# Optimization experiments

Hardware: AMD Instinct MI355X
Metric: run time of the kernel (lower is better)

The kernel has to match this reference:

```python
import jax, jax.numpy as jnp
import numpy as np

N_EXPERTS = 8
TOP_K = 2


def setup_inputs() -> dict:
    key = jax.random.key(0)
    ks = jax.random.split(key, 5)
    B, T, C, E, H = 8, 2048, 256, 8, 682  # H = int(8/3*256)
    scale = 1.0 / np.sqrt(C)
    return {
        "x": jax.random.normal(ks[0], (B, T, C), dtype=jnp.float32),
        "router_w": jax.random.normal(ks[1], (E, C), dtype=jnp.float32) * scale,
        "w1": jax.random.normal(ks[2], (E, H, C), dtype=jnp.float32) * scale,
        "w2": jax.random.normal(ks[3], (E, C, H), dtype=jnp.float32) * (1.0 / np.sqrt(H)),
        "w3": jax.random.normal(ks[4], (E, H, C), dtype=jnp.float32) * scale,
    }


def reference(x, router_w, w1, w2, w3):
    B, T, C = x.shape
    flat = x.reshape(-1, C)  # [N, C]

    # Router: softmax over experts, top-k selection, renormalize.
    logits = flat @ router_w.T                     # [N, E]
    probs = jax.nn.softmax(logits, axis=-1)
    topk_probs, topk_idx = jax.lax.top_k(probs, TOP_K)
    topk_probs = topk_probs / (jnp.sum(topk_probs, axis=-1, keepdims=True) + 1e-9)

    # Dense gate matrix [N, E]: zero for non-selected experts (same math as
    # the masked loop, since unselected experts contribute weight 0).
    onehot = jax.nn.one_hot(topk_idx, N_EXPERTS, dtype=flat.dtype)  # [N, K, E]
    gates = jnp.einsum("nk,nke->ne", topk_probs, onehot)           # [N, E]

    # SwiGLU experts, computed densely over E and combined with gates.
    h1 = jnp.einsum("nc,ehc->neh", flat, w1)       # [N, E, H]
    h3 = jnp.einsum("nc,ehc->neh", flat, w3)       # [N, E, H]
    h = jax.nn.silu(h1) * h3                       # [N, E, H]
    y = jnp.einsum("neh,ech->nec", h, w2)          # [N, E, C]
    out = jnp.einsum("ne,nec->nc", gates, y)       # [N, C]
    return out.reshape(B, T, C)
```

## Files before the change

kernel.cpp:

```cpp
#include <hip/hip_runtime.h>
#include <hip/hip_bf16.h>

#define N_TOK 16384
#define C_DIM 256
#define E_NUM 8
#define H_DIM 682
#define H_PAD 768
#define NROWS (N_TOK * 2)
#define HB 64
#define APB (NROWS / HB)
#define MAXTILE 264

typedef short short8 __attribute__((ext_vector_type(8)));
typedef float floatx4 __attribute__((ext_vector_type(4)));
typedef unsigned int uint;

__device__ inline unsigned short f2bf(float v) {
    union { float f; uint u; } x; x.f = v;
    uint r = (x.u + 0x7fffu + ((x.u >> 16) & 1u)) >> 16;
    return (unsigned short)r;
}
__device__ inline float bf2f(unsigned short v) {
    union { uint u; float f; } x; x.u = ((uint)v) << 16; return x.f;
}
__device__ inline uint pk2(float a, float b) {
    return (uint)f2bf(a) | ((uint)f2bf(b) << 16);
}

__device__ __forceinline__ void load_lds16(const void* g, void* l) {
    __builtin_amdgcn_global_load_lds(
        (const __attribute__((address_space(1))) unsigned int*)g,
        (__attribute__((address_space(3))) unsigned int*)l, 16, 0, 0);
}

#define VMCNT8 asm volatile("s_waitcnt vmcnt(8)" ::: "memory")
#define VMCNT6 asm volatile("s_waitcnt vmcnt(6)" ::: "memory")
#define VMCNT0 asm volatile("s_waitcnt vmcnt(0)" ::: "memory")
#define LGKM0  asm volatile("s_waitcnt lgkmcnt(0)" ::: "memory")

#define P13 (E_NUM * H_PAD * (C_DIM / 2))
#define P2  (E_NUM * C_DIM * (H_PAD / 2))
#define NQUAD ((2 * P13 + P2) / 4)
#define WCONV_BLKS (NQUAD / 256)
#define Q13 (P13 / 4)

__global__ __launch_bounds__(256) void prep_kernel(
    const float* __restrict__ w1, const float* __restrict__ w3, const float* __restrict__ w2,
    unsigned short* __restrict__ w1b, unsigned short* __restrict__ w3b,
    unsigned short* __restrict__ w2b,
    const float* __restrict__ x, const float* __restrict__ rw,
    unsigned short* __restrict__ xb, int* __restrict__ as_e, float* __restrict__ as_gate) {
    __shared__ float rws[E_NUM * C_DIM];
    int tid = threadIdx.x;
    if (blockIdx.x < WCONV_BLKS) {
        int q = blockIdx.x * 256 + tid;
        if (q < 2 * Q13) {
            const float* src = (q < Q13) ? w1 : w3;
            unsigned short* dst = (q < Q13) ? w1b : w3b;
            int i4 = (q < Q13) ? q : q - Q13;
            int e = i4 / (H_PAD * 32);
            int rem = i4 - e * (H_PAD * 32);
            int r = rem >> 5;
            int qc = rem & 31;
            int4 v = {0, 0, 0, 0};
            if (r < H_DIM) {
                const float* s = src + ((size_t)e * H_DIM + r) * C_DIM + qc * 8;
                float4 f0 = *(const float4*)s;
                float4 f1 = *(const float4*)(s + 4);
                v.x = pk2(f0.x, f0.y); v.y = pk2(f0.z, f0.w);
                v.z = pk2(f1.x, f1.y); v.w = pk2(f1.z, f1.w);
            }
            *(int4*)((uint*)dst + (size_t)i4 * 4) = v;
        } else {
            int i4 = q - 2 * Q13;
            int e = i4 / (C_DIM * 96);
            int rem = i4 - e * (C_DIM * 96);
            int r = rem / 96;
            int qc = rem - r * 96;
            const float* s = w2 + ((size_t)e * C_DIM + r) * H_DIM;
            int4 v = {0, 0, 0, 0};
            int j0 = qc * 4;
#pragma unroll
            for (int k = 0; k < 4; k++) {
                int j = j0 + k;
                if (j * 2 < H_DIM) {
                    float2 f = *(const float2*)(s + j * 2);
                    ((uint*)&v)[k] = pk2(f.x, f.y);
                }
            }
            *(int4*)((uint*)w2b + (size_t)i4 * 4) = v;
        }
        return;
    }
    for (int i = tid; i < E_NUM * C_DIM; i += 256) rws[i] = rw[i];
    __syncthreads();
    int wave = tid >> 6, lane = tid & 63;
    int t = (blockIdx.x - WCONV_BLKS) * 4 + wave;
    const float4 xv = *(const float4*)(x + (size_t)t * C_DIM + lane * 4);
    uint2 pk;
    pk.x = pk2(xv.x, xv.y);
    pk.y = pk2(xv.z, xv.w);
    *(uint2*)(xb + (size_t)t * C_DIM + lane * 4) = pk;
    float p[E_NUM];
#pragma unroll
    for (int e = 0; e < E_NUM; e++) {
        const float* wr = &rws[e * C_DIM + lane * 4];
        p[e] = xv.x * wr[0] + xv.y * wr[1] + xv.z * wr[2] + xv.w * wr[3];
    }
#pragma unroll
    for (int off = 32; off >= 1; off >>= 1) {
#pragma unroll
        for (int e = 0; e < E_NUM; e++) p[e] += __shfl_down(p[e], off, 64);
    }
    if (lane == 0) {
        float m = p[0];
#pragma unroll
        for (int e = 1; e < E_NUM; e++) m = fmaxf(m, p[e]);
        float s = 0.f, q[E_NUM];
#pragma unroll
        for (int e = 0; e < E_NUM; e++) { q[e] = expf(p[e] - m); s += q[e]; }
#pragma unroll
        for (int e = 0; e < E_NUM; e++) q[e] /= s;
        int e0 = 0;
#pragma unroll
        for (int e = 1; e < E_NUM; e++) if (q[e] > q[e0]) e0 = e;
        int e1 = (e0 == 0) ? 1 : 0;
#pragma unroll
        for (int e = 0; e < E_NUM; e++) {
            if (e != e0 && q[e] > q[e1]) e1 = e;
        }
        float g0 = q[e0], g1 = q[e1];
        float denom = g0 + g1 + 1e-9f;
        g0 /= denom; g1 /= denom;
        as_e[t * 2] = e0; as_gate[t * 2] = g0;
        as_e[t * 2 + 1] = e1; as_gate[t * 2 + 1] = g1;
    }
}

__global__ __launch_bounds__(256) void hist_kernel(const int* __restrict__ as_e,
                                                   int* __restrict__ block_hist) {
    __shared__ int lh[E_NUM];
    int b = blockIdx.x, tid = threadIdx.x;
    if (tid < E_NUM) lh[tid] = 0;
    __syncthreads();
    for (int i = tid; i < APB; i += 256) atomicAdd(&lh[as_e[b * APB + i]], 1);
    __syncthreads();
    if (tid < E_NUM) block_hist[b * E_NUM + tid] = lh[tid];
}

__global__ void scan2_kernel(const int* __restrict__ block_hist, int* __restrict__ offsets,
                             int* __restrict__ block_base, int* __restrict__ tile_base) {
    __shared__ int tot[E_NUM], off[E_NUM];
    int e = threadIdx.x;
    if (e < E_NUM) {
        int s = 0;
        for (int b = 0; b < HB; b++) s += block_hist[b * E_NUM + e];
        tot[e] = s;
    }
    __syncthreads();
    if (e == 0) {
        int acc = 0;
        for (int i = 0; i < E_NUM; i++) { off[i] = acc; offsets[i] = acc; acc += tot[i]; }
        offsets[E_NUM] = acc;
        int t = 0;
        tile_base[0] = 0;
        for (int i = 0; i < E_NUM; i++) { t += (tot[i] + 127) / 128; tile_base[i + 1] = t; }
    }
    __syncthreads();
    if (e < E_NUM) {
        int acc = off[e];
        for (int b = 0; b < HB; b++) { block_base[b * E_NUM + e] = acc; acc += block_hist[b * E_NUM + e]; }
    }
}

__global__ __launch_bounds__(256) void scatter_kernel(
    const int* __restrict__ as_e, const int* __restrict__ block_base,
    int* __restrict__ row_token, int* __restrict__ as_row) {
    __shared__ int cur[E_NUM];
    int b = blockIdx.x, tid = threadIdx.x;
    if (tid < E_NUM) cur[tid] = block_base[b * E_NUM + tid];
    __syncthreads();
    for (int i = tid; i < APB; i += 256) {
        int a = b * APB + i;
        int e = as_e[a];
        int p = atomicAdd(&cur[e], 1);
        row_token[p] = a >> 1;
        as_row[a] = p;
    }
}

__device__ __forceinline__ int tile_to_expert(const int* __restrict__ tile_base, int bid) {
    int e = 0;
#pragma unroll
    for (int i = 1; i < E_NUM; i++) e += (bid >= tile_base[i]) ? 1 : 0;
    return e;
}

__global__ __launch_bounds__(256, 2) void expert_ffn1(
    const unsigned short* __restrict__ xb, const unsigned short* __restrict__ w1b,
    const unsigned short* __restrict__ w3b, const int* __restrict__ offsets,
    const int* __restrict__ tile_base, const int* __restrict__ row_token,
    unsigned short* __restrict__ h) {
    int bid = blockIdx.x;
    int xcd = bid & 7;
    int local = bid >> 3;
    int tq = local / 6;
    int c = local - tq * 6;
    int t = tq * 8 + xcd;
    if (t >= tile_base[E_NUM]) return;
    int e = tile_to_expert(tile_base, t);
    int mt = t - tile_base[e];
    int off0 = offsets[e], off1 = offsets[e + 1];
    int row0 = off0 + mt * 128;
    int mval = min(128, off1 - row0);

    __shared__ union {
        unsigned short buf[3][12288];
        unsigned short Hs[128 * 136];
    } sm;

    int tid = threadIdx.x, lane = tid & 63, w = tid >> 6;
    int wm = w & 1, wn = w >> 1;
    int ra = tid >> 2;
    int acol = (((tid & 3) ^ ((ra >> 1) & 3))) * 8;
    int tok0 = row_token[row0 + min(ra, mval - 1)];
    int tok1 = row_token[row0 + min(ra + 64, mval - 1)];
    const unsigned short* a0p = xb + (size_t)tok0 * C_DIM + acol;
    const unsigned short* a1p = xb + (size_t)tok1 * C_DIM + acol;
    const unsigned short* b1p0 = w1b + ((size_t)e * H_PAD + c * 128 + ra) * C_DIM + acol;
    const unsigned short* b1p1 = b1p0 + (size_t)64 * C_DIM;
    const unsigned short* b3p0 = w3b + ((size_t)e * H_PAD + c * 128 + ra) * C_DIM + acol;
    const unsigned short* b3p1 = b3p0 + (size_t)64 * C_DIM;

    int wofs = w * 512;
    auto stageA = [&](int kt, unsigned short* base) {
        int kb = kt * 32;
        load_lds16(a0p + kb, base + wofs);
        load_lds16(a1p + kb, base + 2048 + wofs);
        load_lds16(b1p0 + kb, base + 4096 + wofs);
    };
    auto stageB = [&](int kt, unsigned short* base) {
        int kb = kt * 32;
        load_lds16(b1p1 + kb, base + 6144 + wofs);
        load_lds16(b3p0 + kb, base + 8192 + wofs);
        load_lds16(b3p1 + kb, base + 10240 + wofs);
    };

    int ko = ((lane >> 4) ^ ((lane >> 1) & 3)) * 8;
    int l15 = lane & 15;
    int arowf = wm * 64 + l15;
    int browf = wn * 64 + l15;
    int quad = lane >> 4;

    stageA(0, sm.buf[0]); stageB(0, sm.buf[0]);
    stageA(1, sm.buf[1]); stageB(1, sm.buf[1]);

    floatx4 acc1[4][4], acc3[4][4];
#pragma unroll
    for (int m = 0; m < 4; m++)
#pragma unroll
        for (int n = 0; n < 4; n++) {
            acc1[m][n] = (floatx4){0.f, 0.f, 0.f, 0.f};
            acc3[m][n] = (floatx4){0.f, 0.f, 0.f, 0.f};
        }

#pragma unroll
    for (int kt = 0; kt < 8; kt++) {
        if (kt < 7) { VMCNT6; } else { VMCNT0; }
        __builtin_amdgcn_s_barrier();
        const unsigned short* cur = sm.buf[kt % 3];
        unsigned short* nbuf = sm.buf[(kt + 2) % 3];
        short8 af[4], b1f[4], b3f[4];
#pragma unroll
        for (int m = 0; m < 4; m++) af[m] = *(short8*)&cur[(arowf + m * 16) * 32 + ko];
#pragma unroll
        for (int n = 0; n < 4; n++) b1f[n] = *(short8*)&cur[4096 + (browf + n * 16) * 32 + ko];
        if (kt + 2 < 8) stageA(kt + 2, nbuf);
#pragma unroll
        for (int n = 0; n < 4; n++) b3f[n] = *(short8*)&cur[8192 + (browf + n * 16) * 32 + ko];
        __builtin_amdgcn_s_setprio(1);
#pragma unroll
        for (int m = 0; m < 4; m++)
#pragma unroll
            for (int n = 0; n < 4; n++)
                acc1[m][n] = __builtin_amdgcn_mfma_f32_16x16x32_bf16(af[m], b1f[n], acc1[m][n], 0, 0, 0);
        __builtin_amdgcn_s_setprio(0);
        __builtin_amdgcn_s_barrier();
        if (kt + 2 < 8) stageB(kt + 2, nbuf);
        __builtin_amdgcn_s_setprio(1);
#pragma unroll
        for (int m = 0; m < 4; m++)
#pragma unroll
            for (int n = 0; n < 4; n++)
                acc3[m][n] = __builtin_amdgcn_mfma_f32_16x16x32_bf16(af[m], b3f[n], acc3[m][n], 0, 0, 0);
        __builtin_amdgcn_s_setprio(0);
        __builtin_amdgcn_s_barrier();
    }
    __syncthreads();

#pragma unroll
    for (int m = 0; m < 4; m++)
#pragma unroll
        for (int n = 0; n < 4; n++)
#pragma unroll
            for (int r = 0; r < 4; r++) {
                float h1 = acc1[m][n][r], h3 = acc3[m][n][r];
                float sv = h1 / (1.0f + __expf(-h1)) * h3;
                sm.Hs[(wm * 64 + m * 16 + quad * 4 + r) * 136 + wn * 64 + n * 16 + l15] = f2bf(sv);
            }
    __syncthreads();
#pragma unroll
    for (int it = 0; it < 8; it++) {
        int s = it * 256 + tid;
        int row = s >> 4, c16 = s & 15;
        if (row < mval)
            *(int4*)(h + (size_t)(row0 + row) * H_PAD + c * 128 + c16 * 8) =
                *(int4*)&sm.Hs[row * 136 + c16 * 8];
    }
}

__global__ __launch_bounds__(256, 2) void expert_ffn2(
    const unsigned short* __restrict__ h, const unsigned short* __restrict__ w2b,
    const int* __restrict__ offsets, const int* __restrict__ tile_base,
    unsigned short* __restrict__ y) {
    int bid = blockIdx.x;
    int xcd = bid & 7;
    int local = bid >> 3;
    int tq = local >> 1;
    int p = local & 1;
    int t = tq * 8 + xcd;
    if (t >= tile_base[E_NUM]) return;
    int e = tile_to_expert(tile_base, t);
    int mt = t - tile_base[e];
    int off0 = offsets[e], off1 = offsets[e + 1];
    int row0 = off0 + mt * 128;
    int mval = min(128, off1 - row0);

    __shared__ union {
        unsigned short buf[2][16384];
        unsigned short Hs[128 * 136];
    } sm;

    int tid = threadIdx.x, lane = tid & 63, w = tid >> 6;
    int wm = w & 1, wn = w >> 1;
    int ra = tid >> 2;
    int acol = (((tid & 3) ^ ((ra >> 1) & 3))) * 8;
    const unsigned short* ap0 = h + (size_t)(row0 + ra) * H_PAD + acol;
    const unsigned short* ap1 = ap0 + (size_t)64 * H_PAD;
    const unsigned short* bp0 = w2b + ((size_t)e * C_DIM + p * 128 + ra) * H_PAD + acol;
    const unsigned short* bp1 = bp0 + (size_t)64 * H_PAD;

    int wofs = w * 512;
    auto stage = [&](int kt, unsigned short* base) {
        int kb = kt * 64;
#pragma unroll
        for (int kk = 0; kk < 2; kk++) {
            int ks = kb + kk * 32;
            unsigned short* b2 = base + kk * 8192;
            load_lds16(ap0 + ks, b2 + wofs);
            load_lds16(ap1 + ks, b2 + 2048 + wofs);
            load_lds16(bp0 + ks, b2 + 4096 + wofs);
            load_lds16(bp1 + ks, b2 + 6144 + wofs);
        }
    };

    int ko = ((lane >> 4) ^ ((lane >> 1) & 3)) * 8;
    int l15 = lane & 15;
    int arowf = wm * 64 + l15;
    int browf = wn * 64 + l15;
    int quad = lane >> 4;

    stage(0, sm.buf[0]);

    floatx4 acc[4][4];
#pragma unroll
    for (int m = 0; m < 4; m++)
#pragma unroll
        for (int n = 0; n < 4; n++) acc[m][n] = (floatx4){0.f, 0.f, 0.f, 0.f};

#pragma unroll
    for (int kt = 0; kt < H_PAD / 64; kt++) {
        if (kt + 1 < H_PAD / 64) stage(kt + 1, sm.buf[(kt + 1) & 1]);
        if (kt + 1 < H_PAD / 64) { VMCNT8; } else { VMCNT0; }
        __builtin_amdgcn_s_barrier();
        const unsigned short* cur = sm.buf[kt & 1];
#pragma unroll
        for (int kk = 0; kk < 2; kk++) {
            const unsigned short* c2 = cur + kk * 8192;
            short8 af[4], bf[4];
#pragma unroll
            for (int m = 0; m < 4; m++) af[m] = *(short8*)&c2[(arowf + m * 16) * 32 + ko];
#pragma unroll
            for (int n = 0; n < 4; n++) bf[n] = *(short8*)&c2[4096 + (browf + n * 16) * 32 + ko];
            __builtin_amdgcn_s_setprio(1);
#pragma unroll
            for (int m = 0; m < 4; m++)
#pragma unroll
                for (int n = 0; n < 4; n++)
                    acc[m][n] = __builtin_amdgcn_mfma_f32_16x16x32_bf16(af[m], bf[n], acc[m][n], 0, 0, 0);
            __builtin_amdgcn_s_setprio(0);
        }
        LGKM0;
        __builtin_amdgcn_s_barrier();
    }
    __syncthreads();

#pragma unroll
    for (int m = 0; m < 4; m++)
#pragma unroll
        for (int n = 0; n < 4; n++)
#pragma unroll
            for (int r = 0; r < 4; r++)
                sm.Hs[(wm * 64 + m * 16 + quad * 4 + r) * 136 + wn * 64 + n * 16 + l15] =
                    f2bf(acc[m][n][r]);
    __syncthreads();
#pragma unroll
    for (int it = 0; it < 8; it++) {
        int s = it * 256 + tid;
        int row = s >> 4, c16 = s & 15;
        if (row < mval)
            *(int4*)(y + (size_t)(row0 + row) * C_DIM + p * 128 + c16 * 8) =
                *(int4*)&sm.Hs[row * 136 + c16 * 8];
    }
}

__global__ __launch_bounds__(256) void combine_kernel(
    const unsigned short* __restrict__ y, const int* __restrict__ as_row,
    const float* __restrict__ as_gate, float* __restrict__ out) {
    int tid = threadIdx.x, lane = tid & 63;
    int t = blockIdx.x * 4 + (tid >> 6);
    int r0 = as_row[2 * t], r1 = as_row[2 * t + 1];
    float g0 = as_gate[2 * t], g1 = as_gate[2 * t + 1];
    uint2 a = *(const uint2*)(y + (size_t)r0 * C_DIM + lane * 4);
    uint2 b = *(const uint2*)(y + (size_t)r1 * C_DIM + lane * 4);
    float4 o;
    o.x = g0 * bf2f((unsigned short)(a.x & 0xffff)) + g1 * bf2f((unsigned short)(b.x & 0xffff));
    o.y = g0 * bf2f((unsigned short)(a.x >> 16)) + g1 * bf2f((unsigned short)(b.x >> 16));
    o.z = g0 * bf2f((unsigned short)(a.y & 0xffff)) + g1 * bf2f((unsigned short)(b.y & 0xffff));
    o.w = g0 * bf2f((unsigned short)(a.y >> 16)) + g1 * bf2f((unsigned short)(b.y >> 16));
    *(float4*)(out + (size_t)t * C_DIM + lane * 4) = o;
}

extern "C" void kernel_launch(void* const* d_in, const int* in_sizes, int n_in,
                              void* d_out, int out_size, void* d_ws, size_t ws_size,
                              hipStream_t stream) {
    const float* x = (const float*)d_in[0];
    const float* rw = (const float*)d_in[1];
    const float* w1 = (const float*)d_in[2];
    const float* w2 = (const float*)d_in[3];
    const float* w3 = (const float*)d_in[4];
    float* out = (float*)d_out;

    char* ws = (char*)d_ws;
    size_t o = 0;
    auto alloc = [&](size_t bytes) {
        void* p = ws + o;
        o = (o + bytes + 255) & ~(size_t)255;
        return p;
    };
    unsigned short* xb = (unsigned short*)alloc((size_t)N_TOK * C_DIM * 2);
    unsigned short* w1b = (unsigned short*)alloc((size_t)E_NUM * H_PAD * C_DIM * 2);
    unsigned short* w3b = (unsigned short*)alloc((size_t)E_NUM * H_PAD * C_DIM * 2);
    unsigned short* w2b = (unsigned short*)alloc((size_t)E_NUM * C_DIM * H_PAD * 2);
    unsigned short* hbuf = (unsigned short*)alloc((size_t)(NROWS + 128) * H_PAD * 2);
    unsigned short* ybuf = (unsigned short*)alloc((size_t)NROWS * C_DIM * 2);
    int* offsets = (int*)alloc((E_NUM + 1) * 4);
    int* tile_base = (int*)alloc((E_NUM + 1) * 4);
    int* as_e = (int*)alloc(NROWS * 4);
    float* as_gate = (float*)alloc(NROWS * 4);
    int* row_token = (int*)alloc(NROWS * 4);
    int* as_row = (int*)alloc(NROWS * 4);
    int* block_hist = (int*)alloc(HB * E_NUM * 4);
    int* block_base = (int*)alloc(HB * E_NUM * 4);

    prep_kernel<<<WCONV_BLKS + N_TOK / 4, 256, 0, stream>>>(
        w1, w3, w2, w1b, w3b, w2b, x, rw, xb, as_e, as_gate);
    hist_kernel<<<HB, 256, 0, stream>>>(as_e, block_hist);
    scan2_kernel<<<1, 64, 0, stream>>>(block_hist, offsets, block_base, tile_base);
    scatter_kernel<<<HB, 256, 0, stream>>>(as_e, block_base, row_token, as_row);

    expert_ffn1<<<6 * MAXTILE, 256, 0, stream>>>(xb, w1b, w3b, offsets, tile_base,
                                                 row_token, hbuf);
    expert_ffn2<<<2 * MAXTILE, 256, 0, stream>>>(hbuf, w2b, offsets, tile_base, ybuf);
    combine_kernel<<<N_TOK / 4, 256, 0, stream>>>(ybuf, as_row, as_gate, out);
}
```

Measured before the change: 176.9 us.

## Fold scan into scatter kernel and process four tokens per wave in prep

Removes the single-block scan kernel: each scatter block now recomputes the per-expert totals and its own prefix from block_hist, and block 0 writes offsets and tile_base. This drops one kernel launch and the serial scan dependency. Separately, the router/prep blocks now handle four tokens per wave, cutting block count by 4x and amortizing the router-weight LDS load. The cost is redundant prefix work in every scatter block and a longer serial loop per routing block.

```diff
diff --git a/kernel.cpp b/kernel.cpp
--- a/kernel.cpp
+++ b/kernel.cpp
@@ -95,45 +95,49 @@
     for (int i = tid; i < E_NUM * C_DIM; i += 256) rws[i] = rw[i];
     __syncthreads();
     int wave = tid >> 6, lane = tid & 63;
-    int t = (blockIdx.x - WCONV_BLKS) * 4 + wave;
-    const float4 xv = *(const float4*)(x + (size_t)t * C_DIM + lane * 4);
-    uint2 pk;
-    pk.x = pk2(xv.x, xv.y);
-    pk.y = pk2(xv.z, xv.w);
-    *(uint2*)(xb + (size_t)t * C_DIM + lane * 4) = pk;
-    float p[E_NUM];
-#pragma unroll
-    for (int e = 0; e < E_NUM; e++) {
-        const float* wr = &rws[e * C_DIM + lane * 4];
-        p[e] = xv.x * wr[0] + xv.y * wr[1] + xv.z * wr[2] + xv.w * wr[3];
-    }
-#pragma unroll
-    for (int off = 32; off >= 1; off >>= 1) {
-#pragma unroll
-        for (int e = 0; e < E_NUM; e++) p[e] += __shfl_down(p[e], off, 64);
-    }
-    if (lane == 0) {
-        float m = p[0];
-#pragma unroll
-        for (int e = 1; e < E_NUM; e++) m = fmaxf(m, p[e]);
-        float s = 0.f, q[E_NUM];
-#pragma unroll
-        for (int e = 0; e < E_NUM; e++) { q[e] = expf(p[e] - m); s += q[e]; }
-#pragma unroll
-        for (int e = 0; e < E_NUM; e++) q[e] /= s;
-        int e0 = 0;
-#pragma unroll
-        for (int e = 1; e < E_NUM; e++) if (q[e] > q[e0]) e0 = e;
-        int e1 = (e0 == 0) ? 1 : 0;
+    int tbase = (blockIdx.x - WCONV_BLKS) * 16 + wave * 4;
+#pragma unroll
+    for (int tt = 0; tt < 4; tt++) {
+        int t = tbase + tt;
+        const float4 xv = *(const float4*)(x + (size_t)t * C_DIM + lane * 4);
+        uint2 pk;
+        pk.x = pk2(xv.x, xv.y);
+        pk.y = pk2(xv.z, xv.w);
+        *(uint2*)(xb + (size_t)t * C_DIM + lane * 4) = pk;
+        float p[E_NUM];
 #pragma unroll
         for (int e = 0; e < E_NUM; e++) {
-            if (e != e0 && q[e] > q[e1]) e1 = e;
-        }
-        float g0 = q[e0], g1 = q[e1];
-        float denom = g0 + g1 + 1e-9f;
-        g0 /= denom; g1 /= denom;
-        as_e[t * 2] = e0; as_gate[t * 2] = g0;
-        as_e[t * 2 + 1] = e1; as_gate[t * 2 + 1] = g1;
+            const float* wr = &rws[e * C_DIM + lane * 4];
+            p[e] = xv.x * wr[0] + xv.y * wr[1] + xv.z * wr[2] + xv.w * wr[3];
+        }
+#pragma unroll
+        for (int off = 32; off >= 1; off >>= 1) {
+#pragma unroll
+            for (int e = 0; e < E_NUM; e++) p[e] += __shfl_down(p[e], off, 64);
+        }
+        if (lane == 0) {
+            float m = p[0];
+#pragma unroll
+            for (int e = 1; e < E_NUM; e++) m = fmaxf(m, p[e]);
+            float s = 0.f, q[E_NUM];
+#pragma unroll
+            for (int e = 0; e < E_NUM; e++) { q[e] = expf(p[e] - m); s += q[e]; }
+#pragma unroll
+            for (int e = 0; e < E_NUM; e++) q[e] /= s;
+            int e0 = 0;
+#pragma unroll
+            for (int e = 1; e < E_NUM; e++) if (q[e] > q[e0]) e0 = e;
+            int e1 = (e0 == 0) ? 1 : 0;
+#pragma unroll
+            for (int e = 0; e < E_NUM; e++) {
+                if (e != e0 && q[e] > q[e1]) e1 = e;
+            }
+            float g0 = q[e0], g1 = q[e1];
+            float denom = g0 + g1 + 1e-9f;
+            g0 /= denom; g1 /= denom;
+            as_e[t * 2] = e0; as_gate[t * 2] = g0;
+            as_e[t * 2 + 1] = e1; as_gate[t * 2 + 1] = g1;
+        }
     }
 }
 
@@ -148,37 +152,37 @@
     if (tid < E_NUM) block_hist[b * E_NUM + tid] = lh[tid];
 }
 
-__global__ void scan2_kernel(const int* __restrict__ block_hist, int* __restrict__ offsets,
-                             int* __restrict__ block_base, int* __restrict__ tile_base) {
-    __shared__ int tot[E_NUM], off[E_NUM];
-    int e = threadIdx.x;
-    if (e < E_NUM) {
-        int s = 0;
-        for (int b = 0; b < HB; b++) s += block_hist[b * E_NUM + e];
-        tot[e] = s;
-    }
-    __syncthreads();
-    if (e == 0) {
+__global__ __launch_bounds__(256) void scatter_kernel(
+    const int* __restrict__ as_e, const int* __restrict__ block_hist,
+    int* __restrict__ offsets, int* __restrict__ tile_base,
+    int* __restrict__ row_token, int* __restrict__ as_row) {
+    __shared__ int tot_s[E_NUM], pre_s[E_NUM], off_s[E_NUM], cur[E_NUM];
+    int b = blockIdx.x, tid = threadIdx.x;
+    if (tid < E_NUM) {
+        int e = tid, tot = 0, pre = 0;
+        for (int bb = 0; bb < HB; bb++) {
+            int v = block_hist[bb * E_NUM + e];
+            if (bb < b) pre += v;
+            tot += v;
+        }
+        tot_s[e] = tot; pre_s[e] = pre;
+    }
+    __syncthreads();
+    if (tid == 0) {
         int acc = 0;
-        for (int i = 0; i < E_NUM; i++) { off[i] = acc; offsets[i] = acc; acc += tot[i]; }
-        offsets[E_NUM] = acc;
-        int t = 0;
-        tile_base[0] = 0;
-        for (int i = 0; i < E_NUM; i++) { t += (tot[i] + 127) / 128; tile_base[i + 1] = t; }
-    }
-    __syncthreads();
-    if (e < E_NUM) {
-        int acc = off[e];
-        for (int b = 0; b < HB; b++) { block_base[b * E_NUM + e] = acc; acc += block_hist[b * E_NUM + e]; }
-    }
-}
-
-__global__ __launch_bounds__(256) void scatter_kernel(
-    const int* __restrict__ as_e, const int* __restrict__ block_base,
-    int* __restrict__ row_token, int* __restrict__ as_row) {
-    __shared__ int cur[E_NUM];
-    int b = blockIdx.x, tid = threadIdx.x;
-    if (tid < E_NUM) cur[tid] = block_base[b * E_NUM + tid];
+        for (int i = 0; i < E_NUM; i++) { off_s[i] = acc; acc += tot_s[i]; }
+        if (b == 0) {
+            int tb = 0; tile_base[0] = 0;
+            for (int i = 0; i < E_NUM; i++) {
+                offsets[i] = off_s[i];
+                tb += (tot_s[i] + 127) / 128;
+                tile_base[i + 1] = tb;
+            }
+            offsets[E_NUM] = acc;
+        }
+    }
+    __syncthreads();
+    if (tid < E_NUM) cur[tid] = off_s[tid] + pre_s[tid];
     __syncthreads();
     for (int i = tid; i < APB; i += 256) {
         int a = b * APB + i;
@@ -471,13 +475,12 @@
     int* row_token = (int*)alloc(NROWS * 4);
     int* as_row = (int*)alloc(NROWS * 4);
     int* block_hist = (int*)alloc(HB * E_NUM * 4);
-    int* block_base = (int*)alloc(HB * E_NUM * 4);
-
-    prep_kernel<<<WCONV_BLKS + N_TOK / 4, 256, 0, stream>>>(
+
+    prep_kernel<<<WCONV_BLKS + N_TOK / 16, 256, 0, stream>>>(
         w1, w3, w2, w1b, w3b, w2b, x, rw, xb, as_e, as_gate);
     hist_kernel<<<HB, 256, 0, stream>>>(as_e, block_hist);
-    scan2_kernel<<<1, 64, 0, stream>>>(block_hist, offsets, block_base, tile_base);
-    scatter_kernel<<<HB, 256, 0, stream>>>(as_e, block_base, row_token, as_row);
+    scatter_kernel<<<HB, 256, 0, stream>>>(as_e, block_hist, offsets, tile_base,
+                                           row_token, as_row);
 
     expert_ffn1<<<6 * MAXTILE, 256, 0, stream>>>(xb, w1b, w3b, offsets, tile_base,
                                                  row_token, hbuf);
```

Result: slower. 183.7 us (+3.8%).
